# Performance work log

Hardware: AMD Instinct MI355X
Metric: run time of the kernel (lower is better)

Reference implementation:

```python
import jax, jax.numpy as jnp
import numpy as np


def setup_inputs() -> dict:
    key = jax.random.key(0)
    k1, k2, k3 = jax.random.split(key, 3)
    N, C, V, T, K = 32, 64, 25, 1024, 3
    x = jax.random.normal(k1, (N, C, V, T), dtype=jnp.float32)
    # grouped 1x1 conv weight: per node v, maps C -> K*C. torch weight (C*K*V, C, 1, 1)
    W = jax.random.normal(k2, (V, K * C, C), dtype=jnp.float32) * 0.05
    # adjacency buffer A[k, w, v] (src node w -> dst node v, partition k)
    A = jax.random.uniform(k3, (K, V, V), dtype=jnp.float32)
    return {"x": x, "W": W, "A": A}


def reference(x, W, A):
    # x: [N, C, V, T]; W: [V, K*C, C]; A: [K, V, V]
    N, C, V, T = x.shape
    K = A.shape[0]
    # permute(0,2,1,3): [N, V, C, T]; grouped 1x1 conv == per-node matmul C -> K*C
    y = jnp.einsum('ncvt,voc->nvot', x, W)          # [N, V, K*C, T]
    # view (N, V, C*K, T) with output-channel layout o = c*K + k -> split to (C, K)
    y = y.reshape(N, V, C, K, T)                     # [N, V(src=w), C, K, T]
    # einsum('kwv,nckwt->ncvt')
    out = jnp.einsum('kwv,nwckt->ncvt', A, y)        # [N, C, V, T]
    return out
```

## Files before the change

kernel.cpp:

```cpp
#include <hip/hip_runtime.h>

#define Nn 32
#define Cc 64
#define Vv 25
#define Tt 1024

typedef __attribute__((ext_vector_type(4))) float f32x4;
typedef __attribute__((ext_vector_type(8))) short bf16x8;
typedef __attribute__((ext_vector_type(4))) unsigned short u16x4;

__device__ __forceinline__ unsigned short f2bf(float f) {
    union { float f; unsigned u; } a; a.f = f;
    unsigned u = a.u;
    u += 0x7fff + ((u >> 16) & 1);
    return (unsigned short)(u >> 16);
}

__device__ __forceinline__ void gl_lds16(const unsigned short* g, unsigned short* l) {
    __builtin_amdgcn_global_load_lds(
        (const __attribute__((address_space(1))) unsigned int*)g,
        (__attribute__((address_space(3))) unsigned int*)l, 16, 0, 0);
}


__global__ __launch_bounds__(256) void prep_fused(
        const float* __restrict__ x, const float* __restrict__ W,
        const float* __restrict__ A, unsigned short* __restrict__ xb,
        unsigned short* __restrict__ Weff) {
    int bid = blockIdx.x;
    if (bid < Vv * Vv) {
        int v = bid / Vv;
        int w = bid - v * Vv;
        float a0 = A[(0 * Vv + w) * Vv + v];
        float a1 = A[(1 * Vv + w) * Vv + v];
        float a2 = A[(2 * Vv + w) * Vv + v];
        const float* Wb = W + (size_t)w * 192 * 64;
        unsigned short* o = Weff + (size_t)(v * Vv + w) * 4096;
        int c  = threadIdx.x >> 2;
        int c0 = (threadIdx.x & 3) * 16;
        #pragma unroll
        for (int i = 0; i < 16; ++i) {
            int cp = c0 + i;
            float val = a0 * Wb[(c * 3 + 0) * 64 + cp]
                      + a1 * Wb[(c * 3 + 1) * 64 + cp]
                      + a2 * Wb[(c * 3 + 2) * 64 + cp];
            int jl = cp >> 3;
            o[c * 64 + ((jl ^ (c & 7)) << 3) + (cp & 7)] = f2bf(val);
        }
        return;
    }
    int pid = bid - Vv * Vv;
    int n = pid / (Vv * 8);
    int rem = pid - n * (Vv * 8);
    int w = rem >> 3;
    int t0 = (rem & 7) << 7;

    int tid = threadIdx.x;
    int wv = tid >> 6;
    int l  = tid & 63;
    int jl = l & 7;
    int tg = l >> 3;

    int tbase = t0 + wv * 32 + tg * 4;
    const float* xn = x + ((size_t)(n * Cc) * Vv + w) * Tt + tbase;
    unsigned short* dst = xb + ((size_t)(n * Vv + w) * Tt) * 64;

    f32x4 f[8];
    #pragma unroll
    for (int k = 0; k < 8; ++k) {
        int r = jl * 8 + k;
        f[k] = __builtin_nontemporal_load(
            (const f32x4*)(xn + (size_t)r * (Vv * Tt)));
    }
    #pragma unroll
    for (int j = 0; j < 4; ++j) {
        bf16x8 o;
        #pragma unroll
        for (int k = 0; k < 8; ++k) o[k] = (short)f2bf(f[k][j]);
        int tl = tbase + j;
        int pc = jl ^ (tl & 7);
        *(bf16x8*)&dst[(size_t)tl * 64 + pc * 8] = o;
    }
}

__global__ __launch_bounds__(256, 2) void gc_fast(
        const unsigned short* __restrict__ xb,
        const unsigned short* __restrict__ Weff,
        float* __restrict__ out) {
    __shared__ __align__(16) unsigned short wa[4][4096];

    int bid = blockIdx.x;
    int xcd = bid & 7;
    int lid = bid >> 3;
    int v = lid % Vv;
    int s = lid / Vv;
    int slice = (xcd << 4) + s;
    int n  = slice >> 2;
    int t0 = (slice & 3) << 8;

    int tid = threadIdx.x;
    int lane = tid & 63, wv = tid >> 6;
    int m = lane & 15, quad = lane >> 4;

    const unsigned short* wg = Weff + (size_t)v * (Vv * 4096);
    const unsigned short* xbase = xb + ((size_t)(n * Vv) * Tt + t0) * 64;

    int coff0 = ((quad)     ^ (m & 7)) << 3;
    int coff1 = ((4 + quad) ^ (m & 7)) << 3;
    int trow[4], arow[4];
    #pragma unroll
    for (int ni = 0; ni < 4; ++ni) trow[ni] = (wv * 64 + ni * 16 + m) * 64;
    #pragma unroll
    for (int mi = 0; mi < 4; ++mi) arow[mi] = (mi * 16 + m) * 64;

    f32x4 acc[4][4];
    #pragma unroll
    for (int i = 0; i < 4; ++i)
        #pragma unroll
        for (int j = 0; j < 4; ++j)
            acc[i][j] = (f32x4){0.f, 0.f, 0.f, 0.f};

    bf16x8 b0[8], b1[8], b2[8];

#define ISSUE_A(WBUF, w_) do { \
    const unsigned short* s_ = wg + (size_t)(w_) * 4096 + tid * 8; \
    gl_lds16(s_,        &wa[WBUF][tid * 8]); \
    gl_lds16(s_ + 2048, &wa[WBUF][2048 + tid * 8]); \
} while (0)

#define ISSUE_B(BN, w_) do { \
    const unsigned short* xw_ = xbase + (size_t)(w_) * (Tt * 64); \
    _Pragma("unroll") \
    for (int ni_ = 0; ni_ < 4; ++ni_) { \
        BN[ni_]     = *(const bf16x8*)(xw_ + trow[ni_] + coff0); \
        BN[ni_ + 4] = *(const bf16x8*)(xw_ + trow[ni_] + coff1); \
    } \
} while (0)

#define COMPUTE(RBUF, BC) do { \
    const unsigned short* cur_ = &wa[RBUF][0]; \
    bf16x8 af_[8]; \
    _Pragma("unroll") \
    for (int mi_ = 0; mi_ < 4; ++mi_) { \
        af_[mi_]     = *(const bf16x8*)(cur_ + arow[mi_] + coff0); \
        af_[mi_ + 4] = *(const bf16x8*)(cur_ + arow[mi_] + coff1); \
    } \
    __builtin_amdgcn_s_setprio(1); \
    _Pragma("unroll") \
    for (int mi_ = 0; mi_ < 4; ++mi_) \
        _Pragma("unroll") \
        for (int ni_ = 0; ni_ < 4; ++ni_) \
            acc[mi_][ni_] = __builtin_amdgcn_mfma_f32_16x16x32_bf16( \
                af_[mi_], BC[ni_], acc[mi_][ni_], 0, 0, 0); \
    _Pragma("unroll") \
    for (int mi_ = 0; mi_ < 4; ++mi_) \
        _Pragma("unroll") \
        for (int ni_ = 0; ni_ < 4; ++ni_) \
            acc[mi_][ni_] = __builtin_amdgcn_mfma_f32_16x16x32_bf16( \
                af_[mi_ + 4], BC[ni_ + 4], acc[mi_][ni_], 0, 0, 0); \
    __builtin_amdgcn_s_setprio(0); \
} while (0)

#define STEP(RB, WB, BC, BN, w_) do { \
    ISSUE_A(WB, (w_) + 2); \
    ISSUE_B(BN, (w_) + 2); \
    __builtin_amdgcn_sched_barrier(0); \
    asm volatile("s_waitcnt vmcnt(20)" ::: "memory"); \
    __builtin_amdgcn_sched_barrier(0); \
    __builtin_amdgcn_s_barrier(); \
    __builtin_amdgcn_sched_barrier(0); \
    COMPUTE(RB, BC); \
} while (0)

    ISSUE_A(0, 0);
    ISSUE_B(b0, 0);
    ISSUE_A(1, 1);
    ISSUE_B(b1, 1);
    __builtin_amdgcn_sched_barrier(0);

    STEP(0, 2, b0, b2,  0);
    STEP(1, 3, b1, b0,  1);
    STEP(2, 0, b2, b1,  2);
    STEP(3, 1, b0, b2,  3);
    STEP(0, 2, b1, b0,  4);
    STEP(1, 3, b2, b1,  5);
    STEP(2, 0, b0, b2,  6);
    STEP(3, 1, b1, b0,  7);
    STEP(0, 2, b2, b1,  8);
    STEP(1, 3, b0, b2,  9);
    STEP(2, 0, b1, b0, 10);
    STEP(3, 1, b2, b1, 11);
    STEP(0, 2, b0, b2, 12);
    STEP(1, 3, b1, b0, 13);
    STEP(2, 0, b2, b1, 14);
    STEP(3, 1, b0, b2, 15);
    STEP(0, 2, b1, b0, 16);
    STEP(1, 3, b2, b1, 17);
    STEP(2, 0, b0, b2, 18);
    STEP(3, 1, b1, b0, 19);
    STEP(0, 2, b2, b1, 20);
    STEP(1, 3, b0, b2, 21);
    STEP(2, 0, b1, b0, 22);
    asm volatile("s_waitcnt vmcnt(10)" ::: "memory");
    __builtin_amdgcn_sched_barrier(0);
    __builtin_amdgcn_s_barrier();
    __builtin_amdgcn_sched_barrier(0);
    COMPUTE(3, b2);
    asm volatile("s_waitcnt vmcnt(0)" ::: "memory");
    __builtin_amdgcn_sched_barrier(0);
    __builtin_amdgcn_s_barrier();
    __builtin_amdgcn_sched_barrier(0);
    COMPUTE(0, b0);

#undef ISSUE_A
#undef ISSUE_B
#undef COMPUTE
#undef STEP

    float* og = out + ((size_t)n * Cc * Vv + v) * Tt + t0 + wv * 64 + m;
    #pragma unroll
    for (int mi = 0; mi < 4; ++mi)
        #pragma unroll
        for (int r = 0; r < 4; ++r) {
            int c = mi * 16 + quad * 4 + r;
            float* orow = og + (size_t)c * Vv * Tt;
            #pragma unroll
            for (int ni = 0; ni < 4; ++ni)
                __builtin_nontemporal_store(acc[mi][ni][r], &orow[ni * 16]);
        }
}


__global__ __launch_bounds__(256) void weff_prep_plain(
        const float* __restrict__ W, const float* __restrict__ A,
        unsigned short* __restrict__ Weff) {
    int v = blockIdx.x / Vv;
    int w = blockIdx.x - v * Vv;
    float a0 = A[(0 * Vv + w) * Vv + v];
    float a1 = A[(1 * Vv + w) * Vv + v];
    float a2 = A[(2 * Vv + w) * Vv + v];
    const float* Wb = W + (size_t)w * 192 * 64;
    unsigned short* o = Weff + (size_t)(v * Vv + w) * 4096;
    int e0 = threadIdx.x * 16;
    #pragma unroll
    for (int i = 0; i < 16; ++i) {
        int e = e0 + i;
        int c = e >> 6, cp = e & 63;
        float val = a0 * Wb[(c * 3 + 0) * 64 + cp]
                  + a1 * Wb[(c * 3 + 1) * 64 + cp]
                  + a2 * Wb[(c * 3 + 2) * 64 + cp];
        o[e] = f2bf(val);
    }
}

__global__ __launch_bounds__(256, 2) void gc_plain(
        const float* __restrict__ x, const unsigned short* __restrict__ Weff,
        float* __restrict__ out) {
    __shared__ __align__(16) unsigned short xs[256 * 72];
    __shared__ __align__(16) unsigned short wa[64 * 72];
    int bid = blockIdx.x;
    int xcd = bid & 7;
    int lid = bid >> 3;
    int v, s;
    if (lid < 13 * 16) { v = lid % 13;            s = lid / 13; }
    else { int l2 = lid - 13 * 16; v = 13 + l2 % 12; s = l2 / 12; }
    int slice = (xcd << 4) + s;
    int n  = slice >> 2;
    int t0 = (slice & 3) << 8;
    int tid  = threadIdx.x;
    int lane = tid & 63;
    int wv   = tid >> 6;
    int m    = lane & 15;
    int quad = lane >> 4;
    int cc = tid & 7;
    int tt = tid >> 3;
    f32x4 acc[4][4];
    #pragma unroll
    for (int i = 0; i < 4; ++i)
        #pragma unroll
        for (int j = 0; j < 4; ++j)
            acc[i][j] = (f32x4){0.f, 0.f, 0.f, 0.f};
    const float* xg = x + (size_t)n * Cc * Vv * Tt + t0 + tt * 4;
    const bf16x8* wg = (const bf16x8*)(Weff + (size_t)v * Vv * 4096);
    for (int w = 0; w < Vv; ++w) {
        if (w) __syncthreads();
        #pragma unroll
        for (int r = 0; r < 2; ++r) {
            int q = r * 256 + tid;
            int c = q >> 3, b = q & 7;
            *(bf16x8*)&wa[c * 72 + b * 8] = wg[w * 512 + q];
        }
        {
            bf16x8 rows[8];
            #pragma unroll
            for (int i = 0; i < 8; ++i) {
                int cp = cc * 8 + i;
                const float* p = xg + ((size_t)cp * Vv + w) * Tt;
                float4 f0 = *(const float4*)p;
                float4 f1 = *(const float4*)(p + 128);
                rows[0][i] = (short)f2bf(f0.x); rows[1][i] = (short)f2bf(f0.y);
                rows[2][i] = (short)f2bf(f0.z); rows[3][i] = (short)f2bf(f0.w);
                rows[4][i] = (short)f2bf(f1.x); rows[5][i] = (short)f2bf(f1.y);
                rows[6][i] = (short)f2bf(f1.z); rows[7][i] = (short)f2bf(f1.w);
            }
            #pragma unroll
            for (int j = 0; j < 4; ++j) {
                *(bf16x8*)&xs[(tt * 4 + j) * 72 + cc * 8]       = rows[j];
                *(bf16x8*)&xs[(128 + tt * 4 + j) * 72 + cc * 8] = rows[4 + j];
            }
        }
        __syncthreads();
        #pragma unroll
        for (int kc = 0; kc < 2; ++kc) {
            int ko = kc * 32 + quad * 8;
            bf16x8 afr[4], bfr[4];
            #pragma unroll
            for (int mi = 0; mi < 4; ++mi)
                afr[mi] = *(const bf16x8*)&wa[(mi * 16 + m) * 72 + ko];
            #pragma unroll
            for (int ni = 0; ni < 4; ++ni)
                bfr[ni] = *(const bf16x8*)&xs[(wv * 64 + ni * 16 + m) * 72 + ko];
            #pragma unroll
            for (int mi = 0; mi < 4; ++mi)
                #pragma unroll
                for (int ni = 0; ni < 4; ++ni)
                    acc[mi][ni] = __builtin_amdgcn_mfma_f32_16x16x32_bf16(
                        afr[mi], bfr[ni], acc[mi][ni], 0, 0, 0);
        }
    }
    float* og = out + ((size_t)n * Cc * Vv + v) * Tt + t0 + wv * 64 + m;
    #pragma unroll
    for (int mi = 0; mi < 4; ++mi)
        #pragma unroll
        for (int r = 0; r < 4; ++r) {
            int c = mi * 16 + quad * 4 + r;
            float* orow = og + (size_t)c * Vv * Tt;
            #pragma unroll
            for (int ni = 0; ni < 4; ++ni)
                orow[ni * 16] = acc[mi][ni][r];
        }
}

extern "C" void kernel_launch(void* const* d_in, const int* in_sizes, int n_in,
                              void* d_out, int out_size, void* d_ws, size_t ws_size,
                              hipStream_t stream) {
    const float* x = (const float*)d_in[0];
    const float* W = (const float*)d_in[1];
    const float* A = (const float*)d_in[2];
    float* out = (float*)d_out;

    const size_t xb_elems   = (size_t)Nn * Vv * Tt * 64;
    const size_t weff_elems = (size_t)Vv * Vv * 4096;
    const size_t need = (xb_elems + weff_elems) * sizeof(unsigned short);

    if (ws_size >= need) {
        unsigned short* xb   = (unsigned short*)d_ws;
        unsigned short* Weff = xb + xb_elems;
        prep_fused<<<dim3(Vv * Vv + Nn * Vv * 8), dim3(256), 0, stream>>>(x, W, A, xb, Weff);
        gc_fast<<<dim3(3200), dim3(256), 0, stream>>>(xb, Weff, out);
    } else {
        unsigned short* Weff = (unsigned short*)d_ws;
        weff_prep_plain<<<dim3(Vv * Vv), dim3(256), 0, stream>>>(W, A, Weff);
        gc_plain<<<dim3(3200), dim3(256), 0, stream>>>(x, Weff, out);
    }
}
```

Measured before the change: 500.6 us.

## Load Weff A-fragments directly into registers, dropping LDS staging and barriers

The weight (A) tiles were staged into a 4-deep LDS ring via global_load_lds and read back after block barriers. They are now loaded straight from global memory into per-wave registers, double-buffered alongside the x fragments, so the LDS buffers and all s_barriers go away. Compute now comes before the next issue inside each step. Each wave fetches its own copy of the shared weight tile, which multiplies weight global/L2 traffic by four and raises register use. The vmcnt waits are retuned for the new load counts.

New measurement: 558.8 us. 1.12x slower.

```diff
diff --git a/kernel.cpp b/kernel.cpp
--- a/kernel.cpp
+++ b/kernel.cpp
@@ -14,12 +14,6 @@
     unsigned u = a.u;
     u += 0x7fff + ((u >> 16) & 1);
     return (unsigned short)(u >> 16);
-}
-
-__device__ __forceinline__ void gl_lds16(const unsigned short* g, unsigned short* l) {
-    __builtin_amdgcn_global_load_lds(
-        (const __attribute__((address_space(1))) unsigned int*)g,
-        (__attribute__((address_space(3))) unsigned int*)l, 16, 0, 0);
 }
 
 
@@ -87,8 +81,6 @@
         const unsigned short* __restrict__ xb,
         const unsigned short* __restrict__ Weff,
         float* __restrict__ out) {
-    __shared__ __align__(16) unsigned short wa[4][4096];
-
     int bid = blockIdx.x;
     int xcd = bid & 7;
     int lid = bid >> 3;
@@ -120,100 +112,84 @@
         for (int j = 0; j < 4; ++j)
             acc[i][j] = (f32x4){0.f, 0.f, 0.f, 0.f};
 
-    bf16x8 b0[8], b1[8], b2[8];
-
-#define ISSUE_A(WBUF, w_) do { \
-    const unsigned short* s_ = wg + (size_t)(w_) * 4096 + tid * 8; \
-    gl_lds16(s_,        &wa[WBUF][tid * 8]); \
-    gl_lds16(s_ + 2048, &wa[WBUF][2048 + tid * 8]); \
-} while (0)
-
-#define ISSUE_B(BN, w_) do { \
+    bf16x8 aA[8], bA[8], aB[8], bB[8];
+
+#define ISSUE(AR, BR, w_) do { \
+    const unsigned short* aw_ = wg + (size_t)(w_) * 4096; \
     const unsigned short* xw_ = xbase + (size_t)(w_) * (Tt * 64); \
     _Pragma("unroll") \
+    for (int mi_ = 0; mi_ < 4; ++mi_) { \
+        AR[mi_]     = *(const bf16x8*)(aw_ + arow[mi_] + coff0); \
+        AR[mi_ + 4] = *(const bf16x8*)(aw_ + arow[mi_] + coff1); \
+    } \
+    _Pragma("unroll") \
     for (int ni_ = 0; ni_ < 4; ++ni_) { \
-        BN[ni_]     = *(const bf16x8*)(xw_ + trow[ni_] + coff0); \
-        BN[ni_ + 4] = *(const bf16x8*)(xw_ + trow[ni_] + coff1); \
+        BR[ni_]     = *(const bf16x8*)(xw_ + trow[ni_] + coff0); \
+        BR[ni_ + 4] = *(const bf16x8*)(xw_ + trow[ni_] + coff1); \
     } \
 } while (0)
 
-#define COMPUTE(RBUF, BC) do { \
-    const unsigned short* cur_ = &wa[RBUF][0]; \
-    bf16x8 af_[8]; \
-    _Pragma("unroll") \
-    for (int mi_ = 0; mi_ < 4; ++mi_) { \
-        af_[mi_]     = *(const bf16x8*)(cur_ + arow[mi_] + coff0); \
-        af_[mi_ + 4] = *(const bf16x8*)(cur_ + arow[mi_] + coff1); \
-    } \
+#define COMPUTE(AC, BC) do { \
     __builtin_amdgcn_s_setprio(1); \
     _Pragma("unroll") \
     for (int mi_ = 0; mi_ < 4; ++mi_) \
         _Pragma("unroll") \
         for (int ni_ = 0; ni_ < 4; ++ni_) \
             acc[mi_][ni_] = __builtin_amdgcn_mfma_f32_16x16x32_bf16( \
-                af_[mi_], BC[ni_], acc[mi_][ni_], 0, 0, 0); \
+                AC[mi_], BC[ni_], acc[mi_][ni_], 0, 0, 0); \
     _Pragma("unroll") \
     for (int mi_ = 0; mi_ < 4; ++mi_) \
         _Pragma("unroll") \
         for (int ni_ = 0; ni_ < 4; ++ni_) \
             acc[mi_][ni_] = __builtin_amdgcn_mfma_f32_16x16x32_bf16( \
-                af_[mi_ + 4], BC[ni_ + 4], acc[mi_][ni_], 0, 0, 0); \
+                AC[mi_ + 4], BC[ni_ + 4], acc[mi_][ni_], 0, 0, 0); \
     __builtin_amdgcn_s_setprio(0); \
 } while (0)
 
-#define STEP(RB, WB, BC, BN, w_) do { \
-    ISSUE_A(WB, (w_) + 2); \
-    ISSUE_B(BN, (w_) + 2); \
+#define STEP(AC, BC, w_) do { \
+    asm volatile("s_waitcnt vmcnt(16)" ::: "memory"); \
     __builtin_amdgcn_sched_barrier(0); \
-    asm volatile("s_waitcnt vmcnt(20)" ::: "memory"); \
+    COMPUTE(AC, BC); \
     __builtin_amdgcn_sched_barrier(0); \
-    __builtin_amdgcn_s_barrier(); \
+    ISSUE(AC, BC, (w_) + 2); \
     __builtin_amdgcn_sched_barrier(0); \
-    COMPUTE(RB, BC); \
 } while (0)
 
-    ISSUE_A(0, 0);
-    ISSUE_B(b0, 0);
-    ISSUE_A(1, 1);
-    ISSUE_B(b1, 1);
+    ISSUE(aA, bA, 0);
+    ISSUE(aB, bB, 1);
     __builtin_amdgcn_sched_barrier(0);
 
-    STEP(0, 2, b0, b2,  0);
-    STEP(1, 3, b1, b0,  1);
-    STEP(2, 0, b2, b1,  2);
-    STEP(3, 1, b0, b2,  3);
-    STEP(0, 2, b1, b0,  4);
-    STEP(1, 3, b2, b1,  5);
-    STEP(2, 0, b0, b2,  6);
-    STEP(3, 1, b1, b0,  7);
-    STEP(0, 2, b2, b1,  8);
-    STEP(1, 3, b0, b2,  9);
-    STEP(2, 0, b1, b0, 10);
-    STEP(3, 1, b2, b1, 11);
-    STEP(0, 2, b0, b2, 12);
-    STEP(1, 3, b1, b0, 13);
-    STEP(2, 0, b2, b1, 14);
-    STEP(3, 1, b0, b2, 15);
-    STEP(0, 2, b1, b0, 16);
-    STEP(1, 3, b2, b1, 17);
-    STEP(2, 0, b0, b2, 18);
-    STEP(3, 1, b1, b0, 19);
-    STEP(0, 2, b2, b1, 20);
-    STEP(1, 3, b0, b2, 21);
-    STEP(2, 0, b1, b0, 22);
-    asm volatile("s_waitcnt vmcnt(10)" ::: "memory");
+    STEP(aA, bA,  0);
+    STEP(aB, bB,  1);
+    STEP(aA, bA,  2);
+    STEP(aB, bB,  3);
+    STEP(aA, bA,  4);
+    STEP(aB, bB,  5);
+    STEP(aA, bA,  6);
+    STEP(aB, bB,  7);
+    STEP(aA, bA,  8);
+    STEP(aB, bB,  9);
+    STEP(aA, bA, 10);
+    STEP(aB, bB, 11);
+    STEP(aA, bA, 12);
+    STEP(aB, bB, 13);
+    STEP(aA, bA, 14);
+    STEP(aB, bB, 15);
+    STEP(aA, bA, 16);
+    STEP(aB, bB, 17);
+    STEP(aA, bA, 18);
+    STEP(aB, bB, 19);
+    STEP(aA, bA, 20);
+    STEP(aB, bB, 21);
+    STEP(aA, bA, 22);
+    asm volatile("s_waitcnt vmcnt(16)" ::: "memory");
     __builtin_amdgcn_sched_barrier(0);
-    __builtin_amdgcn_s_barrier();
-    __builtin_amdgcn_sched_barrier(0);
-    COMPUTE(3, b2);
+    COMPUTE(aB, bB);
     asm volatile("s_waitcnt vmcnt(0)" ::: "memory");
     __builtin_amdgcn_sched_barrier(0);
-    __builtin_amdgcn_s_barrier();
-    __builtin_amdgcn_sched_barrier(0);
-    COMPUTE(0, b0);
-
-#undef ISSUE_A
-#undef ISSUE_B
+    COMPUTE(aA, bA);
+
+#undef ISSUE
 #undef COMPUTE
 #undef STEP
 
```

## Deepen Weff LDS ring to 8 stages and halve block barriers per step

Applied to the files above, without the earlier changes.

The shared-memory ring for the A (Weff) tiles grows from 4 to 8 buffers, and the main loop is restructured into double-steps that prefetch A tiles four ahead and issue one s_barrier per two node iterations instead of per iteration. B register loads are split so the second iteration's loads are issued between the two compute phases. The aim is to cut barrier stalls and hide more global load latency. The cost is double the LDS per block (64 KB), which may limit occupancy at 2 blocks per CU, and hand-tuned vmcnt counts that must exactly match the issue order to stay correct.

Measured after the change: 501.5 us. About the same (+0.2%).

```diff
diff --git a/kernel.cpp b/kernel.cpp
--- a/kernel.cpp
+++ b/kernel.cpp
@@ -87,7 +87,7 @@
         const unsigned short* __restrict__ xb,
         const unsigned short* __restrict__ Weff,
         float* __restrict__ out) {
-    __shared__ __align__(16) unsigned short wa[4][4096];
+    __shared__ __align__(16) unsigned short wa[8][4096];
 
     int bid = blockIdx.x;
     int xcd = bid & 7;
@@ -120,7 +120,10 @@
         for (int j = 0; j < 4; ++j)
             acc[i][j] = (f32x4){0.f, 0.f, 0.f, 0.f};
 
-    bf16x8 b0[8], b1[8], b2[8];
+    bf16x8 b0v[8], b1v[8], b2v[8];
+
+#define SB __builtin_amdgcn_sched_barrier(0)
+#define VMCNT(N_) asm volatile("s_waitcnt vmcnt(" #N_ ")" ::: "memory")
 
 #define ISSUE_A(WBUF, w_) do { \
     const unsigned short* s_ = wg + (size_t)(w_) * 4096 + tid * 8; \
@@ -137,7 +140,7 @@
     } \
 } while (0)
 
-#define COMPUTE(RBUF, BC) do { \
+#define COMP(RBUF, BC) do { \
     const unsigned short* cur_ = &wa[RBUF][0]; \
     bf16x8 af_[8]; \
     _Pragma("unroll") \
@@ -161,61 +164,73 @@
     __builtin_amdgcn_s_setprio(0); \
 } while (0)
 
-#define STEP(RB, WB, BC, BN, w_) do { \
-    ISSUE_A(WB, (w_) + 2); \
-    ISSUE_B(BN, (w_) + 2); \
-    __builtin_amdgcn_sched_barrier(0); \
-    asm volatile("s_waitcnt vmcnt(20)" ::: "memory"); \
-    __builtin_amdgcn_sched_barrier(0); \
+#define DSTEP(R0, R1, W4, W5, C0, C1, I2, I3, w_, N3, N6) do { \
+    ISSUE_B(I2, (w_) + 2); \
+    ISSUE_A(W4, (w_) + 4); \
+    ISSUE_A(W5, (w_) + 5); \
+    SB; VMCNT(N3); SB; \
     __builtin_amdgcn_s_barrier(); \
-    __builtin_amdgcn_sched_barrier(0); \
-    COMPUTE(RB, BC); \
+    SB; \
+    COMP(R0, C0); \
+    SB; \
+    ISSUE_B(I3, (w_) + 3); \
+    SB; VMCNT(N6); SB; \
+    COMP(R1, C1); \
+    SB; \
 } while (0)
 
+    ISSUE_B(b0v, 0);
+    ISSUE_B(b1v, 1);
     ISSUE_A(0, 0);
-    ISSUE_B(b0, 0);
     ISSUE_A(1, 1);
-    ISSUE_B(b1, 1);
-    __builtin_amdgcn_sched_barrier(0);
-
-    STEP(0, 2, b0, b2,  0);
-    STEP(1, 3, b1, b0,  1);
-    STEP(2, 0, b2, b1,  2);
-    STEP(3, 1, b0, b2,  3);
-    STEP(0, 2, b1, b0,  4);
-    STEP(1, 3, b2, b1,  5);
-    STEP(2, 0, b0, b2,  6);
-    STEP(3, 1, b1, b0,  7);
-    STEP(0, 2, b2, b1,  8);
-    STEP(1, 3, b0, b2,  9);
-    STEP(2, 0, b1, b0, 10);
-    STEP(3, 1, b2, b1, 11);
-    STEP(0, 2, b0, b2, 12);
-    STEP(1, 3, b1, b0, 13);
-    STEP(2, 0, b2, b1, 14);
-    STEP(3, 1, b0, b2, 15);
-    STEP(0, 2, b1, b0, 16);
-    STEP(1, 3, b2, b1, 17);
-    STEP(2, 0, b0, b2, 18);
-    STEP(3, 1, b1, b0, 19);
-    STEP(0, 2, b2, b1, 20);
-    STEP(1, 3, b0, b2, 21);
-    STEP(2, 0, b1, b0, 22);
-    asm volatile("s_waitcnt vmcnt(10)" ::: "memory");
-    __builtin_amdgcn_sched_barrier(0);
+    ISSUE_A(2, 2);
+    ISSUE_A(3, 3);
+    SB;
+
+    DSTEP(0, 1, 4, 5, b0v, b1v, b2v, b0v,  0, 16, 20);
+    DSTEP(2, 3, 6, 7, b2v, b0v, b1v, b2v,  2, 24, 20);
+    DSTEP(4, 5, 0, 1, b1v, b2v, b0v, b1v,  4, 24, 20);
+    DSTEP(6, 7, 2, 3, b0v, b1v, b2v, b0v,  6, 24, 20);
+    DSTEP(0, 1, 4, 5, b2v, b0v, b1v, b2v,  8, 24, 20);
+    DSTEP(2, 3, 6, 7, b1v, b2v, b0v, b1v, 10, 24, 20);
+    DSTEP(4, 5, 0, 1, b0v, b1v, b2v, b0v, 12, 24, 20);
+    DSTEP(6, 7, 2, 3, b2v, b0v, b1v, b2v, 14, 24, 20);
+    DSTEP(0, 1, 4, 5, b1v, b2v, b0v, b1v, 16, 24, 20);
+    DSTEP(2, 3, 6, 7, b0v, b1v, b2v, b0v, 18, 24, 20);
+
+    ISSUE_B(b1v, 22);
+    ISSUE_A(0, 24);
+    SB; VMCNT(22); SB;
     __builtin_amdgcn_s_barrier();
-    __builtin_amdgcn_sched_barrier(0);
-    COMPUTE(3, b2);
-    asm volatile("s_waitcnt vmcnt(0)" ::: "memory");
-    __builtin_amdgcn_sched_barrier(0);
+    SB;
+    COMP(4, b2v);
+    SB;
+    ISSUE_B(b2v, 23);
+    SB; VMCNT(18); SB;
+    COMP(5, b0v);
+    SB;
+
+    ISSUE_B(b0v, 24);
+    SB; VMCNT(18); SB;
     __builtin_amdgcn_s_barrier();
-    __builtin_amdgcn_sched_barrier(0);
-    COMPUTE(0, b0);
-
+    SB;
+    COMP(6, b1v);
+    SB; VMCNT(10); SB;
+    COMP(7, b2v);
+    SB;
+
+    VMCNT(0);
+    SB;
+    __builtin_amdgcn_s_barrier();
+    SB;
+    COMP(0, b0v);
+
+#undef DSTEP
+#undef COMP
+#undef ISSUE_B
 #undef ISSUE_A
-#undef ISSUE_B
-#undef COMPUTE
-#undef STEP
+#undef VMCNT
+#undef SB
 
     float* og = out + ((size_t)n * Cc * Vv + v) * Tt + t0 + wv * 64 + m;
     #pragma unroll
```
